# Optimization experiments

Measured on AMD Instinct MI355X. Metric: run time of the kernel, lower is better.

## Reference

```python
import jax, jax.numpy as jnp
import numpy as np

DEPTH = 3


def _outer(a, b):
    # batched tensor product of flattened tensor-algebra levels: (B, m) x (B, n) -> (B, m*n)
    return (a[:, :, None] * b[:, None, :]).reshape(a.shape[0], -1)


def _signature(X, depth):
    """Truncated path signature via Chen's identity (matches signatory.signature,
    basepoint=False). X: (B, T, C) -> (B, sum_k C^k)."""
    B, T, C = X.shape
    dX = X[:, 1:, :] - X[:, :-1, :]  # (B, T-1, C) increments

    def exp_levels(dx):
        # exp(dx) in truncated tensor algebra: level k = dx^{\otimes k} / k!
        e = [dx]
        for k in range(2, depth + 1):
            e.append(_outer(e[-1], dx) / k)
        return e

    def step(S, dx):
        e = exp_levels(dx)
        new = []
        for k in range(1, depth + 1):
            t = S[k - 1] + e[k - 1]  # terms with S_0=1 or e_0=1
            for i in range(1, k):
                t = t + _outer(S[i - 1], e[k - i - 1])
            new.append(t)
        return tuple(new), None

    init = tuple(jnp.zeros((B, C ** k), X.dtype) for k in range(1, depth + 1))
    S, _ = jax.lax.scan(step, init, jnp.swapaxes(dX, 0, 1))  # scan over time
    return jnp.concatenate(S, axis=1)


def setup_inputs() -> dict:
    key = jax.random.key(0)
    kx, kw, kb = jax.random.split(key, 3)
    B, T, C, n_out = 2048, 128, 8, 10
    sig_dim = sum(C ** k for k in range(1, DEPTH + 1))  # 584
    X = jax.random.normal(kx, (B, T, C), dtype=jnp.float32)
    bound = 1.0 / np.sqrt(sig_dim)
    W = jax.random.uniform(kw, (n_out, sig_dim), jnp.float32, -bound, bound)
    b = jax.random.uniform(kb, (n_out,), jnp.float32, -bound, bound)
    return {"X": X, "W": W, "b": b}


def reference(X, W, b):
    sig = _signature(X, DEPTH)          # (B, sig_dim)
    out = sig @ W.T + b                  # (B, n_outputs)
    return out.reshape(-1, W.shape[0])
```

## Files before the change

### kernel.cpp

```cpp
#include <hip/hip_runtime.h>

#define NOUT 10
#define SIG_DIM 584
#define TPAD 132

__device__ __forceinline__ float rdlane(float x, int lane) {
    return __int_as_float(__builtin_amdgcn_readlane(__float_as_int(x), lane));
}

__global__ __launch_bounds__(256) void sig_linear_kernel(
    const float* __restrict__ X, const float* __restrict__ W,
    const float* __restrict__ bias, float* __restrict__ out)
{
    __shared__ float s_dxT[4][8 * TPAD];

    const int tid = threadIdx.x;
    const int w = tid >> 6;
    const int l = tid & 63;
    const int i = l >> 3;
    const int j = l & 7;
    const int b = blockIdx.x * 4 + w;

    const float* Xb = X + (size_t)b * 1024;
    float* dxT = &s_dxT[w][0];
    const int cb = (l & 1) * 4;
    const int rl = l >> 1;

    float4 dA, dB, dC, dD;
#define PREP(DQ, QQ)                                                          \
    {                                                                         \
        const int r = (QQ) * 32 + rl;                                         \
        const float* xr = Xb + r * 8 + cb;                                    \
        const float4 a  = *reinterpret_cast<const float4*>(xr);               \
        const float4 c4 = *reinterpret_cast<const float4*>(xr + (r < 127 ? 8 : 0)); \
        DQ.x = (r < 127) ? c4.x - a.x : 0.f;                                  \
        DQ.y = (r < 127) ? c4.y - a.y : 0.f;                                  \
        DQ.z = (r < 127) ? c4.z - a.z : 0.f;                                  \
        DQ.w = (r < 127) ? c4.w - a.w : 0.f;                                  \
        dxT[(cb + 0) * TPAD + r] = DQ.x;                                      \
        dxT[(cb + 1) * TPAD + r] = DQ.y;                                      \
        dxT[(cb + 2) * TPAD + r] = DQ.z;                                      \
        dxT[(cb + 3) * TPAD + r] = DQ.w;                                      \
    }
    PREP(dA, 0) PREP(dB, 1) PREP(dC, 2) PREP(dD, 3)
#undef PREP
    __syncthreads();

    float s3[8];
#pragma unroll
    for (int k = 0; k < 8; ++k) s3[k] = 0.f;
    float s2 = 0.f, s1i = 0.f, s1j = 0.f;

    const float* icol = dxT + i * TPAD;
    const float* jcol = dxT + j * TPAD;

#define STEP(DQ, LB, DXI, DXJ)                                                \
    {                                                                         \
        const float k0 = rdlane(DQ.x, (LB));                                  \
        const float k1 = rdlane(DQ.y, (LB));                                  \
        const float k2 = rdlane(DQ.z, (LB));                                  \
        const float k3 = rdlane(DQ.w, (LB));                                  \
        const float k4 = rdlane(DQ.x, (LB) + 1);                              \
        const float k5 = rdlane(DQ.y, (LB) + 1);                              \
        const float k6 = rdlane(DQ.z, (LB) + 1);                              \
        const float k7 = rdlane(DQ.w, (LB) + 1);                              \
        const float cc = (DXI) * (DXJ);                                       \
        const float uu = s1i * (DXJ);                                         \
        const float f  = fmaf(0.5f, uu, fmaf(1.0f / 6.0f, cc, s2));           \
        s3[0] = fmaf(f, k0, s3[0]);                                           \
        s3[1] = fmaf(f, k1, s3[1]);                                           \
        s3[2] = fmaf(f, k2, s3[2]);                                           \
        s3[3] = fmaf(f, k3, s3[3]);                                           \
        s3[4] = fmaf(f, k4, s3[4]);                                           \
        s3[5] = fmaf(f, k5, s3[5]);                                           \
        s3[6] = fmaf(f, k6, s3[6]);                                           \
        s3[7] = fmaf(f, k7, s3[7]);                                           \
        s2 = fmaf(0.5f, cc, s2 + uu);                                         \
        s1i += (DXI);                                                         \
        s1j += (DXJ);                                                         \
    }

#define SECTION(DQ, QQ)                                                       \
    for (int g = 0; g < 8; ++g) {                                             \
        const int t0 = (QQ) * 32 + g * 4;                                     \
        const float4 ic = *reinterpret_cast<const float4*>(icol + t0);        \
        const float4 jc = *reinterpret_cast<const float4*>(jcol + t0);        \
        const int lb = g * 8;                                                 \
        STEP(DQ, lb + 0, ic.x, jc.x)                                          \
        STEP(DQ, lb + 2, ic.y, jc.y)                                          \
        STEP(DQ, lb + 4, ic.z, jc.z)                                          \
        STEP(DQ, lb + 6, ic.w, jc.w)                                          \
    }
    SECTION(dA, 0)
    SECTION(dB, 1)
    SECTION(dC, 2)
    SECTION(dD, 3)
#undef SECTION
#undef STEP

#pragma unroll
    for (int o = 0; o < NOUT; ++o) {
        const float* wrow = W + o * SIG_DIM;
        float part = s2 * wrow[8 + l];
        const float4 w0 = *reinterpret_cast<const float4*>(wrow + 72 + l * 8);
        const float4 w1 = *reinterpret_cast<const float4*>(wrow + 72 + l * 8 + 4);
        part = fmaf(s3[0], w0.x, part); part = fmaf(s3[1], w0.y, part);
        part = fmaf(s3[2], w0.z, part); part = fmaf(s3[3], w0.w, part);
        part = fmaf(s3[4], w1.x, part); part = fmaf(s3[5], w1.y, part);
        part = fmaf(s3[6], w1.z, part); part = fmaf(s3[7], w1.w, part);
        if (i == 0) part = fmaf(s1j, wrow[j], part);
#pragma unroll
        for (int off = 32; off > 0; off >>= 1) part += __shfl_xor(part, off);
        if (l == 0) out[b * NOUT + o] = part + bias[o];
    }
}

extern "C" void kernel_launch(void* const* d_in, const int* in_sizes, int n_in,
                              void* d_out, int out_size, void* d_ws, size_t ws_size,
                              hipStream_t stream) {
    const float* X = (const float*)d_in[0];
    const float* W = (const float*)d_in[1];
    const float* bias = (const float*)d_in[2];
    float* out = (float*)d_out;
    sig_linear_kernel<<<dim3(512), dim3(256), 0, stream>>>(X, W, bias, out);
}
```

Measured before the change: 21.60 us.

## Split each path's time scan across two wavefronts and merge via Chen identity

Each batch element is now handled by two wavefronts, each scanning half of the time steps, so the serial dependency chain per wave is halved. The two partial signatures are exchanged through shared memory and combined with Chen's identity. The output projection is also split between the two waves by output index. The grid doubles to keep one path per pair of waves, at the cost of extra shared memory, a second block barrier and a small combine step.

```diff
diff --git a/kernel.cpp b/kernel.cpp
--- a/kernel.cpp
+++ b/kernel.cpp
@@ -2,7 +2,7 @@
 
 #define NOUT 10
 #define SIG_DIM 584
-#define TPAD 132
+#define TPAD 68
 
 __device__ __forceinline__ float rdlane(float x, int lane) {
     return __int_as_float(__builtin_amdgcn_readlane(__float_as_int(x), lane));
@@ -13,23 +13,28 @@
     const float* __restrict__ bias, float* __restrict__ out)
 {
     __shared__ float s_dxT[4][8 * TPAD];
+    __shared__ float s_sig[4][SIG_DIM];
 
     const int tid = threadIdx.x;
     const int w = tid >> 6;
     const int l = tid & 63;
     const int i = l >> 3;
     const int j = l & 7;
-    const int b = blockIdx.x * 4 + w;
+    const int p = w >> 1;
+    const int ch = w & 1;
+    const int b = blockIdx.x * 2 + p;
 
     const float* Xb = X + (size_t)b * 1024;
     float* dxT = &s_dxT[w][0];
     const int cb = (l & 1) * 4;
     const int rl = l >> 1;
+    const int R0 = ch * 64;
 
-    float4 dA, dB, dC, dD;
+    float4 dA, dB;
 #define PREP(DQ, QQ)                                                          \
     {                                                                         \
-        const int r = (QQ) * 32 + rl;                                         \
+        const int r  = R0 + (QQ) * 32 + rl;                                   \
+        const int lr = (QQ) * 32 + rl;                                        \
         const float* xr = Xb + r * 8 + cb;                                    \
         const float4 a  = *reinterpret_cast<const float4*>(xr);               \
         const float4 c4 = *reinterpret_cast<const float4*>(xr + (r < 127 ? 8 : 0)); \
@@ -37,12 +42,12 @@
         DQ.y = (r < 127) ? c4.y - a.y : 0.f;                                  \
         DQ.z = (r < 127) ? c4.z - a.z : 0.f;                                  \
         DQ.w = (r < 127) ? c4.w - a.w : 0.f;                                  \
-        dxT[(cb + 0) * TPAD + r] = DQ.x;                                      \
-        dxT[(cb + 1) * TPAD + r] = DQ.y;                                      \
-        dxT[(cb + 2) * TPAD + r] = DQ.z;                                      \
-        dxT[(cb + 3) * TPAD + r] = DQ.w;                                      \
+        dxT[(cb + 0) * TPAD + lr] = DQ.x;                                     \
+        dxT[(cb + 1) * TPAD + lr] = DQ.y;                                     \
+        dxT[(cb + 2) * TPAD + lr] = DQ.z;                                     \
+        dxT[(cb + 3) * TPAD + lr] = DQ.w;                                     \
     }
-    PREP(dA, 0) PREP(dB, 1) PREP(dC, 2) PREP(dD, 3)
+    PREP(dA, 0) PREP(dB, 1)
 #undef PREP
     __syncthreads();
 
@@ -93,13 +98,48 @@
     }
     SECTION(dA, 0)
     SECTION(dB, 1)
-    SECTION(dC, 2)
-    SECTION(dD, 3)
 #undef SECTION
 #undef STEP
 
+    {
+        float* sg = s_sig[w];
+        if (i == 0) sg[j] = s1j;
+        sg[8 + l] = s2;
 #pragma unroll
-    for (int o = 0; o < NOUT; ++o) {
+        for (int k = 0; k < 8; ++k) sg[72 + k * 64 + l] = s3[k];
+    }
+    __syncthreads();
+
+#pragma unroll
+    for (int k = 0; k < 8; ++k) s3[k] = 0.f;
+    s2 = 0.f; s1i = 0.f; s1j = 0.f;
+#pragma unroll
+    for (int c = 0; c < 2; ++c) {
+        const float* sg = s_sig[p * 2 + c];
+        const float4 b0 = *reinterpret_cast<const float4*>(sg);
+        const float4 b1 = *reinterpret_cast<const float4*>(sg + 4);
+        const float s1bi = sg[i];
+        const float s1bj = sg[j];
+        const float s2b = sg[8 + l];
+        const float4 q0 = *reinterpret_cast<const float4*>(sg + 8 + j * 8);
+        const float4 q1 = *reinterpret_cast<const float4*>(sg + 8 + j * 8 + 4);
+        float tb[8];
+#pragma unroll
+        for (int k = 0; k < 8; ++k) tb[k] = sg[72 + k * 64 + l];
+        s3[0] = fmaf(s2, b0.x, fmaf(s1i, q0.x, s3[0] + tb[0]));
+        s3[1] = fmaf(s2, b0.y, fmaf(s1i, q0.y, s3[1] + tb[1]));
+        s3[2] = fmaf(s2, b0.z, fmaf(s1i, q0.z, s3[2] + tb[2]));
+        s3[3] = fmaf(s2, b0.w, fmaf(s1i, q0.w, s3[3] + tb[3]));
+        s3[4] = fmaf(s2, b1.x, fmaf(s1i, q1.x, s3[4] + tb[4]));
+        s3[5] = fmaf(s2, b1.y, fmaf(s1i, q1.y, s3[5] + tb[5]));
+        s3[6] = fmaf(s2, b1.z, fmaf(s1i, q1.z, s3[6] + tb[6]));
+        s3[7] = fmaf(s2, b1.w, fmaf(s1i, q1.w, s3[7] + tb[7]));
+        s2 = s2 + fmaf(s1i, s1bj, s2b);
+        s1i += s1bi;
+        s1j += s1bj;
+    }
+
+    for (int o = ch; o < NOUT; o += 2) {
         const float* wrow = W + o * SIG_DIM;
         float part = s2 * wrow[8 + l];
         const float4 w0 = *reinterpret_cast<const float4*>(wrow + 72 + l * 8);
@@ -122,5 +162,5 @@
     const float* W = (const float*)d_in[1];
     const float* bias = (const float*)d_in[2];
     float* out = (float*)d_out;
-    sig_linear_kernel<<<dim3(512), dim3(256), 0, stream>>>(X, W, bias, out);
+    sig_linear_kernel<<<dim3(1024), dim3(256), 0, stream>>>(X, W, bias, out);
 }
```

Measured after the change: 27.54 us, median of 2. +27.5%, slower.

## Precompute increments in workspace prepass and read rows via scalar loads

Applied to the files above, without the earlier changes.

Adds a separate prepass kernel that writes the time increments of X into a workspace buffer. The main kernel then reads each full 8-wide increment row through a wave-uniform pointer, which the compiler can serve with scalar loads, instead of broadcasting values with readlane from VGPRs. Level-1 sums are taken from the path endpoints rather than accumulated. The aim is to take the readlane traffic out of the inner loop, at the cost of a second launch and an extra 8 MB write and read through global memory. The original kernel is kept as a fallback when the workspace is too small.

```diff
diff --git a/kernel.cpp b/kernel.cpp
--- a/kernel.cpp
+++ b/kernel.cpp
@@ -4,13 +4,31 @@
 #define SIG_DIM 584
 #define TPAD 132
 
+typedef float float8v __attribute__((ext_vector_type(8)));
+
 __device__ __forceinline__ float rdlane(float x, int lane) {
     return __int_as_float(__builtin_amdgcn_readlane(__float_as_int(x), lane));
 }
 
-__global__ __launch_bounds__(256) void sig_linear_kernel(
-    const float* __restrict__ X, const float* __restrict__ W,
-    const float* __restrict__ bias, float* __restrict__ out)
+__global__ __launch_bounds__(256) void dx_prepass(const float* __restrict__ X,
+                                                  float* __restrict__ dX)
+{
+    const int t = blockIdx.x * 256 + threadIdx.x;
+    const int r = (t >> 1) & 127;
+    const float4* X4 = reinterpret_cast<const float4*>(X);
+    const float4 a = X4[t];
+    float4 d = make_float4(0.f, 0.f, 0.f, 0.f);
+    if (r < 127) {
+        const float4 c = X4[t + 2];
+        d = make_float4(c.x - a.x, c.y - a.y, c.z - a.z, c.w - a.w);
+    }
+    reinterpret_cast<float4*>(dX)[t] = d;
+}
+
+__global__ __launch_bounds__(256) void sig_main(
+    const float* __restrict__ X, const float* __restrict__ dX,
+    const float* __restrict__ W, const float* __restrict__ bias,
+    float* __restrict__ out)
 {
     __shared__ float s_dxT[4][8 * TPAD];
 
@@ -20,12 +38,100 @@
     const int i = l >> 3;
     const int j = l & 7;
     const int b = blockIdx.x * 4 + w;
-
+    const int bu = __builtin_amdgcn_readfirstlane(b);
+    const float* dXb = dX + (size_t)bu * 1024;
+
+    float* dxT = &s_dxT[w][0];
+    const int cb = (l & 1) * 4;
+    const int rl = l >> 1;
+#pragma unroll
+    for (int q = 0; q < 4; ++q) {
+        const int r = q * 32 + rl;
+        const float4 d = *reinterpret_cast<const float4*>(dXb + r * 8 + cb);
+        dxT[(cb + 0) * TPAD + r] = d.x;
+        dxT[(cb + 1) * TPAD + r] = d.y;
+        dxT[(cb + 2) * TPAD + r] = d.z;
+        dxT[(cb + 3) * TPAD + r] = d.w;
+    }
+    __syncthreads();
+
+    float s3[8];
+#pragma unroll
+    for (int k = 0; k < 8; ++k) s3[k] = 0.f;
+    float s2 = 0.f, s1i = 0.f;
+
+    const float* icol = dxT + i * TPAD;
+    const float* jcol = dxT + j * TPAD;
+    const float8v* srow = reinterpret_cast<const float8v*>(dXb);
+
+#define STEP(T, DXI, DXJ)                                                     \
+    {                                                                         \
+        const float8v rr = srow[(T)];              \
+        const float cc = (DXI) * (DXJ);                                       \
+        const float uu = s1i * (DXJ);                                         \
+        const float f  = fmaf(0.5f, uu, fmaf(1.0f / 6.0f, cc, s2));           \
+        s3[0] = fmaf(f, rr[0], s3[0]);                                        \
+        s3[1] = fmaf(f, rr[1], s3[1]);                                        \
+        s3[2] = fmaf(f, rr[2], s3[2]);                                        \
+        s3[3] = fmaf(f, rr[3], s3[3]);                                        \
+        s3[4] = fmaf(f, rr[4], s3[4]);                                        \
+        s3[5] = fmaf(f, rr[5], s3[5]);                                        \
+        s3[6] = fmaf(f, rr[6], s3[6]);                                        \
+        s3[7] = fmaf(f, rr[7], s3[7]);                                        \
+        s2 = fmaf(0.5f, cc, s2 + uu);                                         \
+        s1i += (DXI);                                                         \
+    }
+
+#define GROUP(T0)                                                             \
+    {                                                                         \
+        const float4 ic = *reinterpret_cast<const float4*>(icol + (T0));      \
+        const float4 jc = *reinterpret_cast<const float4*>(jcol + (T0));      \
+        STEP((T0) + 0, ic.x, jc.x)                                            \
+        STEP((T0) + 1, ic.y, jc.y)                                            \
+        STEP((T0) + 2, ic.z, jc.z)                                            \
+        STEP((T0) + 3, ic.w, jc.w)                                            \
+    }
+#define G16(A) GROUP(A) GROUP((A) + 4) GROUP((A) + 8) GROUP((A) + 12)
+    G16(0) G16(16) G16(32) G16(48) G16(64) G16(80) G16(96) G16(112)
+#undef G16
+#undef GROUP
+#undef STEP
+
+    const float* Xb = X + (size_t)b * 1024;
+    const float s1j = Xb[127 * 8 + j] - Xb[j];
+
+#pragma unroll
+    for (int o = 0; o < NOUT; ++o) {
+        const float* wrow = W + o * SIG_DIM;
+        float part = s2 * wrow[8 + l];
+        const float4 w0 = *reinterpret_cast<const float4*>(wrow + 72 + l * 8);
+        const float4 w1 = *reinterpret_cast<const float4*>(wrow + 72 + l * 8 + 4);
+        part = fmaf(s3[0], w0.x, part); part = fmaf(s3[1], w0.y, part);
+        part = fmaf(s3[2], w0.z, part); part = fmaf(s3[3], w0.w, part);
+        part = fmaf(s3[4], w1.x, part); part = fmaf(s3[5], w1.y, part);
+        part = fmaf(s3[6], w1.z, part); part = fmaf(s3[7], w1.w, part);
+        if (i == 0) part = fmaf(s1j, wrow[j], part);
+#pragma unroll
+        for (int off = 32; off > 0; off >>= 1) part += __shfl_xor(part, off);
+        if (l == 0) out[b * NOUT + o] = part + bias[o];
+    }
+}
+
+__global__ __launch_bounds__(256) void sig_fallback(
+    const float* __restrict__ X, const float* __restrict__ W,
+    const float* __restrict__ bias, float* __restrict__ out)
+{
+    __shared__ float s_dxT[4][8 * TPAD];
+    const int tid = threadIdx.x;
+    const int w = tid >> 6;
+    const int l = tid & 63;
+    const int i = l >> 3;
+    const int j = l & 7;
+    const int b = blockIdx.x * 4 + w;
     const float* Xb = X + (size_t)b * 1024;
     float* dxT = &s_dxT[w][0];
     const int cb = (l & 1) * 4;
     const int rl = l >> 1;
-
     float4 dA, dB, dC, dD;
 #define PREP(DQ, QQ)                                                          \
     {                                                                         \
@@ -45,15 +151,12 @@
     PREP(dA, 0) PREP(dB, 1) PREP(dC, 2) PREP(dD, 3)
 #undef PREP
     __syncthreads();
-
     float s3[8];
 #pragma unroll
     for (int k = 0; k < 8; ++k) s3[k] = 0.f;
     float s2 = 0.f, s1i = 0.f, s1j = 0.f;
-
     const float* icol = dxT + i * TPAD;
     const float* jcol = dxT + j * TPAD;
-
 #define STEP(DQ, LB, DXI, DXJ)                                                \
     {                                                                         \
         const float k0 = rdlane(DQ.x, (LB));                                  \
@@ -79,7 +182,6 @@
         s1i += (DXI);                                                         \
         s1j += (DXJ);                                                         \
     }
-
 #define SECTION(DQ, QQ)                                                       \
     for (int g = 0; g < 8; ++g) {                                             \
         const int t0 = (QQ) * 32 + g * 4;                                     \
@@ -91,13 +193,9 @@
         STEP(DQ, lb + 4, ic.z, jc.z)                                          \
         STEP(DQ, lb + 6, ic.w, jc.w)                                          \
     }
-    SECTION(dA, 0)
-    SECTION(dB, 1)
-    SECTION(dC, 2)
-    SECTION(dD, 3)
+    SECTION(dA, 0) SECTION(dB, 1) SECTION(dC, 2) SECTION(dD, 3)
 #undef SECTION
 #undef STEP
-
 #pragma unroll
     for (int o = 0; o < NOUT; ++o) {
         const float* wrow = W + o * SIG_DIM;
@@ -122,5 +220,12 @@
     const float* W = (const float*)d_in[1];
     const float* bias = (const float*)d_in[2];
     float* out = (float*)d_out;
-    sig_linear_kernel<<<dim3(512), dim3(256), 0, stream>>>(X, W, bias, out);
-}
+    const size_t need = 2048ull * 1024ull * sizeof(float);
+    if (ws_size >= need) {
+        float* dX = (float*)d_ws;
+        dx_prepass<<<dim3(2048), dim3(256), 0, stream>>>(X, dX);
+        sig_main<<<dim3(512), dim3(256), 0, stream>>>(X, dX, W, bias, out);
+    } else {
+        sig_fallback<<<dim3(512), dim3(256), 0, stream>>>(X, W, bias, out);
+    }
+}
```

After: 25.17 us. 16.5% more time.

## Split each batch row's level-3 accumulation across two wavefronts

Applied to the files above, without the earlier changes.

Each batch element is now handled by two wavefronts, each owning half of the level-3 signature components (4 instead of 8 accumulators per lane). Grid size doubles, and the partial linear outputs are combined through shared memory after a block barrier. The level-1 signature is computed directly as the endpoint difference instead of being accumulated, and the inner group loop is explicitly unrolled. In exchange, both wavefronts redundantly build the transposed increments and recompute the level-2 terms, and the second shared-memory barrier adds synchronisation.

```diff
diff --git a/kernel.cpp b/kernel.cpp
--- a/kernel.cpp
+++ b/kernel.cpp
@@ -13,13 +13,15 @@
     const float* __restrict__ bias, float* __restrict__ out)
 {
     __shared__ float s_dxT[4][8 * TPAD];
+    __shared__ float s_part[4][16];
 
     const int tid = threadIdx.x;
     const int w = tid >> 6;
     const int l = tid & 63;
     const int i = l >> 3;
     const int j = l & 7;
-    const int b = blockIdx.x * 4 + w;
+    const int h = w & 1;
+    const int b = blockIdx.x * 2 + (w >> 1);
 
     const float* Xb = X + (size_t)b * 1024;
     float* dxT = &s_dxT[w][0];
@@ -46,24 +48,19 @@
 #undef PREP
     __syncthreads();
 
-    float s3[8];
-#pragma unroll
-    for (int k = 0; k < 8; ++k) s3[k] = 0.f;
-    float s2 = 0.f, s1i = 0.f, s1j = 0.f;
+    float s3[4];
+    s3[0] = s3[1] = s3[2] = s3[3] = 0.f;
+    float s2 = 0.f, s1i = 0.f;
 
     const float* icol = dxT + i * TPAD;
     const float* jcol = dxT + j * TPAD;
 
 #define STEP(DQ, LB, DXI, DXJ)                                                \
     {                                                                         \
-        const float k0 = rdlane(DQ.x, (LB));                                  \
-        const float k1 = rdlane(DQ.y, (LB));                                  \
-        const float k2 = rdlane(DQ.z, (LB));                                  \
-        const float k3 = rdlane(DQ.w, (LB));                                  \
-        const float k4 = rdlane(DQ.x, (LB) + 1);                              \
-        const float k5 = rdlane(DQ.y, (LB) + 1);                              \
-        const float k6 = rdlane(DQ.z, (LB) + 1);                              \
-        const float k7 = rdlane(DQ.w, (LB) + 1);                              \
+        const float k0 = rdlane(DQ.x, (LB) + h);                              \
+        const float k1 = rdlane(DQ.y, (LB) + h);                              \
+        const float k2 = rdlane(DQ.z, (LB) + h);                              \
+        const float k3 = rdlane(DQ.w, (LB) + h);                              \
         const float cc = (DXI) * (DXJ);                                       \
         const float uu = s1i * (DXJ);                                         \
         const float f  = fmaf(0.5f, uu, fmaf(1.0f / 6.0f, cc, s2));           \
@@ -71,16 +68,12 @@
         s3[1] = fmaf(f, k1, s3[1]);                                           \
         s3[2] = fmaf(f, k2, s3[2]);                                           \
         s3[3] = fmaf(f, k3, s3[3]);                                           \
-        s3[4] = fmaf(f, k4, s3[4]);                                           \
-        s3[5] = fmaf(f, k5, s3[5]);                                           \
-        s3[6] = fmaf(f, k6, s3[6]);                                           \
-        s3[7] = fmaf(f, k7, s3[7]);                                           \
         s2 = fmaf(0.5f, cc, s2 + uu);                                         \
         s1i += (DXI);                                                         \
-        s1j += (DXJ);                                                         \
     }
 
 #define SECTION(DQ, QQ)                                                       \
+    _Pragma("unroll")                                                         \
     for (int g = 0; g < 8; ++g) {                                             \
         const int t0 = (QQ) * 32 + g * 4;                                     \
         const float4 ic = *reinterpret_cast<const float4*>(icol + t0);        \
@@ -91,28 +84,31 @@
         STEP(DQ, lb + 4, ic.z, jc.z)                                          \
         STEP(DQ, lb + 6, ic.w, jc.w)                                          \
     }
-    SECTION(dA, 0)
-    SECTION(dB, 1)
-    SECTION(dC, 2)
-    SECTION(dD, 3)
+    SECTION(dA, 0) SECTION(dB, 1) SECTION(dC, 2) SECTION(dD, 3)
 #undef SECTION
 #undef STEP
+
+    const float s1j = Xb[127 * 8 + j] - Xb[j];
 
 #pragma unroll
     for (int o = 0; o < NOUT; ++o) {
         const float* wrow = W + o * SIG_DIM;
-        float part = s2 * wrow[8 + l];
-        const float4 w0 = *reinterpret_cast<const float4*>(wrow + 72 + l * 8);
-        const float4 w1 = *reinterpret_cast<const float4*>(wrow + 72 + l * 8 + 4);
-        part = fmaf(s3[0], w0.x, part); part = fmaf(s3[1], w0.y, part);
-        part = fmaf(s3[2], w0.z, part); part = fmaf(s3[3], w0.w, part);
-        part = fmaf(s3[4], w1.x, part); part = fmaf(s3[5], w1.y, part);
-        part = fmaf(s3[6], w1.z, part); part = fmaf(s3[7], w1.w, part);
-        if (i == 0) part = fmaf(s1j, wrow[j], part);
+        const float4 w0 = *reinterpret_cast<const float4*>(wrow + 72 + l * 8 + h * 4);
+        float part = fmaf(s3[0], w0.x,
+                     fmaf(s3[1], w0.y,
+                     fmaf(s3[2], w0.z, s3[3] * w0.w)));
+        if (h == 0) {
+            part = fmaf(s2, wrow[8 + l], part);
+            if (i == 0) part = fmaf(s1j, wrow[j], part);
+        }
 #pragma unroll
         for (int off = 32; off > 0; off >>= 1) part += __shfl_xor(part, off);
-        if (l == 0) out[b * NOUT + o] = part + bias[o];
+        if (l == o) s_part[w][o] = part;
     }
+    __syncthreads();
+
+    if (h == 0 && l < NOUT)
+        out[b * NOUT + l] = s_part[w][l] + s_part[w + 1][l] + bias[l];
 }
 
 extern "C" void kernel_launch(void* const* d_in, const int* in_sizes, int n_in,
@@ -122,5 +118,5 @@
     const float* W = (const float*)d_in[1];
     const float* bias = (const float*)d_in[2];
     float* out = (float*)d_out;
-    sig_linear_kernel<<<dim3(512), dim3(256), 0, stream>>>(X, W, bias, out);
+    sig_linear_kernel<<<dim3(1024), dim3(256), 0, stream>>>(X, W, bias, out);
 }
```

New measurement: 29.69 us. 37.5% more time.
